# Kernel optimization log

Measured on AMD Instinct MI355X. Metric: run time of the kernel, lower is better.

## Reference

```python
import jax, jax.numpy as jnp
import numpy as np

BETA = 0.05      # temperature
BG_KNN = 50      # hard negatives per sample
N_CAMS = 6
C = 2000         # classes (proxies) per camera
D = 2048         # feature dim
B = 256          # batch size
MASK_VAL = -10000.0


def setup_inputs() -> dict:
    key = jax.random.key(0)
    k1, k2, k3, k4 = jax.random.split(key, 4)
    feats = jax.random.normal(k1, (B, D), jnp.float32)
    feats = feats / jnp.linalg.norm(feats, axis=1, keepdims=True)
    mem = jax.random.normal(k2, (N_CAMS, C, D), jnp.float32)
    mem = mem / jnp.linalg.norm(mem, axis=2, keepdims=True)
    cams = jax.random.randint(k3, (B,), 0, N_CAMS)
    labels = jax.random.randint(k4, (B,), 0, C)
    return {"features": feats, "memory": mem, "cams": cams, "labels": labels}


def _forward(features, memory, cams, labels):
    # Memory bank is non-differentiable in ExemplarMemory (grad only flows to inputs).
    mem_flat = jax.lax.stop_gradient(memory.reshape(N_CAMS * C, D))
    # [B, N_CAMS*C] similarities against the concatenated per-camera proxies (percam_tempV)
    sims_all = features @ mem_flat.T

    rows = jnp.arange(B)
    counts = jax.ops.segment_sum(jnp.ones((B,), sims_all.dtype), cams, num_segments=N_CAMS)
    safe_counts = jnp.maximum(counts, 1.0)

    # ---- per-camera proxy cross-entropy (ExemplarMemory forward + F.cross_entropy) ----
    # camera cc owns memory rows cc*C : (cc+1)*C; gather each sample's own-camera block
    block_idx = cams[:, None] * C + jnp.arange(C)[None, :]            # [B, C]
    percam_logits = jnp.take_along_axis(sims_all, block_idx, axis=1) / BETA
    ce = -jax.nn.log_softmax(percam_logits, axis=1)[rows, labels]     # [B]
    ce_sum = jax.ops.segment_sum(ce, cams, num_segments=N_CAMS)
    # original sums the per-camera *mean* CE over cameras present in the batch
    loss = jnp.sum(jnp.where(counts > 0, ce_sum / safe_counts, 0.0))

    # ---- cross-camera associate loss: positives + bg_knn hardest negatives ----
    # positives of label l live at global rows {j*C + l} for every camera j
    pos_idx = labels[:, None] + C * jnp.arange(N_CAMS)[None, :]       # [B, N_CAMS]
    temp_sims = jax.lax.stop_gradient(sims_all)
    temp_sims = temp_sims.at[rows[:, None], pos_idx].set(MASK_VAL)    # mask positives
    _, sel_idx = jax.lax.top_k(temp_sims, BG_KNN)                     # [B, BG_KNN] hard negs
    neg_logits = jnp.take_along_axis(sims_all, sel_idx, axis=1) / BETA
    pos_logits = jnp.take_along_axis(sims_all, pos_idx, axis=1) / BETA
    logits = jnp.concatenate([pos_logits, neg_logits], axis=1)       # [B, N_CAMS+BG_KNN]
    logsm = jax.nn.log_softmax(logits, axis=1)
    # soft target: uniform 1/n_pos mass on the positive slots
    assoc = -jnp.sum(logsm[:, :N_CAMS], axis=1) / N_CAMS              # [B]
    assoc_sum = jax.ops.segment_sum(assoc, cams, num_segments=N_CAMS)
    loss = loss + jnp.sum(jnp.where(counts > 0, 0.5 * assoc_sum / safe_counts, 0.0))
    return loss


def reference(features, memory, cams, labels):
    return _forward(features, memory, cams, labels)
```

## Files before the change

kernel.cpp:

```cpp
#include <hip/hip_runtime.h>
#include <hip/hip_bf16.h>
#include <math.h>

#define BETA_INV 20.0f
#define BG_KNN   50
#define N_CAMS   6
#define CLS      2000
#define DIM      2048
#define BATCH    256
#define NPROXY   (N_CAMS * CLS)
#define MASK_VAL -10000.0f
#define NKT      (DIM / 32)

typedef __attribute__((ext_vector_type(8))) short short8;
typedef __attribute__((ext_vector_type(4))) float f32x4;
typedef __attribute__((address_space(1))) const unsigned int g_u32;
typedef __attribute__((address_space(3))) unsigned int l_u32;

__device__ __forceinline__ uint2 cvt4(float4 v) {
    uint2 r;
    asm("v_cvt_pk_bf16_f32 %0, %1, %2" : "=v"(r.x) : "v"(v.x), "v"(v.y));
    asm("v_cvt_pk_bf16_f32 %0, %1, %2" : "=v"(r.y) : "v"(v.z), "v"(v.w));
    return r;
}

__global__ __launch_bounds__(256) void conv_t(const float* __restrict__ src,
                                              unsigned short* __restrict__ dst,
                                              int nrb)
{
    __shared__ unsigned short lds[32][72];
    const int t  = threadIdx.x;
    const int b  = blockIdx.x;
    const int rb = b % nrb, kb = b / nrb;
    const int r  = t >> 3, c8 = (t & 7) * 8;

    const float* sp = src + (size_t)(rb * 32 + r) * DIM + kb * 64 + c8;
    float4 f0 = *(const float4*)sp;
    float4 f1 = *(const float4*)(sp + 4);
    uint2 pa = cvt4(f0), pb = cvt4(f1);
    *(uint4*)&lds[r][c8] = make_uint4(pa.x, pa.y, pb.x, pb.y);
    __syncthreads();

    const int cidx = t >> 6;
    const int n16h = cidx >> 1, kth = cidx & 1;
    const int lane = t & 63;
    const int fr = lane & 15, kg = lane >> 4;
    uint4 v = *(const uint4*)&lds[n16h * 16 + fr][kth * 32 + kg * 8];
    const size_t N16 = (size_t)rb * 2 + n16h;
    const size_t KT  = (size_t)kb * 2 + kth;
    *(uint4*)(dst + ((N16 * NKT + KT) * 64 + lane) * 8) = v;
}

#define NSTEP 16

__global__ __launch_bounds__(512, 2) void gemm_fused(const unsigned short* __restrict__ At,
                                                     const float* __restrict__ Bm,
                                                     float* __restrict__ C)
{
    __shared__ __align__(16) unsigned short ldsA[2][16384];
    __shared__ __align__(16) float          ldsB[2][6144];

    const int tid = threadIdx.x;
    const int bid = blockIdx.x;
    const int bn  = (bid >> 1) * 96;
    const int kh  = bid & 1;

    const int lane = tid & 63, wid = tid >> 6;
    const int mw = wid >> 1;
    const int nw = wid & 1;
    const int fr = lane & 15, kg = lane >> 4;

    const unsigned short* pAq[4];
    int dA[4];
#pragma unroll
    for (int q = 0; q < 4; ++q) {
        int f = q * 512 + tid;
        int chunk = f >> 6, ln = f & 63;
        int n16 = chunk >> 1, ktl = chunk & 1;
        pAq[q] = At + ((size_t)(n16 * 64 + kh * 32 + ktl) * 64 + ln) * 8;
        dA[q] = f * 8;
    }
    const float* pBq[3];
    int dB[3];
#pragma unroll
    for (int q = 0; q < 3; ++q) {
        int f = q * 512 + tid;
        int row = f >> 4, c = f & 15;
        pBq[q] = Bm + (size_t)(bn + row) * DIM + kh * 1024 + ((c ^ (row & 15)) * 4);
        dB[q] = f * 4;
    }

#define STAGE(BUF, T) do {                                                                \
        _Pragma("unroll")                                                                 \
        for (int q = 0; q < 4; ++q)                                                       \
            __builtin_amdgcn_global_load_lds((g_u32*)(pAq[q] + (size_t)(T) * 1024),       \
                                             (l_u32*)&ldsA[BUF][dA[q]], 16, 0, 0);        \
        _Pragma("unroll")                                                                 \
        for (int q = 0; q < 3; ++q)                                                       \
            __builtin_amdgcn_global_load_lds((g_u32*)(pBq[q] + (size_t)(T) * 64),         \
                                             (l_u32*)&ldsB[BUF][dB[q]], 16, 0, 0);        \
    } while (0)

    f32x4 acc[4][3];
#pragma unroll
    for (int i = 0; i < 4; ++i)
#pragma unroll
        for (int j = 0; j < 3; ++j) acc[i][j] = (f32x4){0.f, 0.f, 0.f, 0.f};

#define COMPUTE(CUR) do {                                                                 \
    _Pragma("unroll")                                                                     \
    for (int ks = 0; ks < 2; ++ks) {                                                      \
        short8 bfr[3];                                                                    \
        _Pragma("unroll")                                                                 \
        for (int j = 0; j < 3; ++j) {                                                     \
            int row = nw * 48 + j * 16 + fr;                                              \
            int g0 = ks * 8 + kg * 2;                                                     \
            float4 lo = *(const float4*)&ldsB[CUR][row * 64 + ((g0 ^ fr) * 4)];           \
            float4 hi = *(const float4*)&ldsB[CUR][row * 64 + (((g0 + 1) ^ fr) * 4)];     \
            uint2 ca = cvt4(lo), cb = cvt4(hi);                                           \
            bfr[j] = __builtin_bit_cast(short8, make_uint4(ca.x, ca.y, cb.x, cb.y));      \
        }                                                                                 \
        _Pragma("unroll")                                                                 \
        for (int i = 0; i < 4; ++i) {                                                     \
            short8 af = *(const short8*)&ldsA[CUR][((mw * 4 + i) * 2 + ks) * 512 + lane * 8]; \
            _Pragma("unroll")                                                             \
            for (int j = 0; j < 3; ++j)                                                   \
                acc[i][j] = __builtin_amdgcn_mfma_f32_16x16x32_bf16(af, bfr[j], acc[i][j], 0, 0, 0); \
        }                                                                                 \
    }                                                                                     \
} while (0)

#define BODY(T, CUR, ISSUE, VMC) do {                                                     \
    __builtin_amdgcn_s_barrier();                   \
    __builtin_amdgcn_sched_barrier(0);                                                    \
    if (ISSUE) { STAGE((CUR) ^ 1, (T) + 1); }                                             \
    __builtin_amdgcn_sched_barrier(0);                                                    \
    asm volatile("s_waitcnt vmcnt(" VMC ")" ::: "memory");         \
    __builtin_amdgcn_sched_barrier(0);                                                    \
    __builtin_amdgcn_s_barrier();                           \
    __builtin_amdgcn_sched_barrier(0);                                                    \
    COMPUTE(CUR);                                                                         \
} while (0)

    STAGE(0, 0);
#pragma unroll 1
    for (int t = 0; t < NSTEP - 2; t += 2) {
        BODY(t,     0, 1, "7");
        BODY(t + 1, 1, 1, "7");
    }
    BODY(NSTEP - 2, 0, 1, "7");
    BODY(NSTEP - 1, 1, 0, "0");
#undef BODY
#undef COMPUTE
#undef STAGE

    float* Cp = C + (size_t)kh * BATCH * NPROXY;
#pragma unroll
    for (int i = 0; i < 4; ++i)
#pragma unroll
        for (int j = 0; j < 3; ++j)
#pragma unroll
            for (int r = 0; r < 4; ++r)
                Cp[(size_t)(mw * 64 + i * 16 + kg * 4 + r) * NPROXY + (bn + nw * 48 + j * 16 + fr)] = acc[i][j][r];
}

__device__ __forceinline__ float block_sum_f(float x, volatile float* red8, int lane, int wid) {
#pragma unroll
    for (int off = 32; off; off >>= 1) x += __shfl_xor(x, off);
    if (lane == 0) red8[wid] = x;
    __syncthreads();
    float t = 0.f;
#pragma unroll
    for (int w = 0; w < 8; ++w) t += red8[w];
    __syncthreads();
    return t;
}
__device__ __forceinline__ float block_max_f(float x, volatile float* red8, int lane, int wid) {
#pragma unroll
    for (int off = 32; off; off >>= 1) x = fmaxf(x, __shfl_xor(x, off));
    if (lane == 0) red8[wid] = x;
    __syncthreads();
    float t = -1e30f;
#pragma unroll
    for (int w = 0; w < 8; ++w) t = fmaxf(t, red8[w]);
    __syncthreads();
    return t;
}
__device__ __forceinline__ int block_sum_i(int x, volatile int* red8, int lane, int wid) {
#pragma unroll
    for (int off = 32; off; off >>= 1) x += __shfl_xor(x, off);
    if (lane == 0) red8[wid] = x;
    __syncthreads();
    int t = 0;
#pragma unroll
    for (int w = 0; w < 8; ++w) t += red8[w];
    __syncthreads();
    return t;
}

__global__ __launch_bounds__(512) void per_sample(const float* __restrict__ sims,
                                                  const int* __restrict__ cams,
                                                  const int* __restrict__ labels,
                                                  float* __restrict__ ce_out,
                                                  float* __restrict__ assoc_out)
{
    __shared__ float redf[8];
    __shared__ int   redi[8];
    __shared__ float pos_sh[N_CAMS];
    __shared__ float sh_vlab;

    const int i    = blockIdx.x;
    const int tid  = threadIdx.x;
    const int lane = tid & 63;
    const int wid  = tid >> 6;
    const float* s0 = sims + (size_t)i * NPROXY;
    const float* s1 = sims + (size_t)(BATCH + i) * NPROXY;
    const int cc   = cams[i];
    const int lab  = labels[i];

    float4 v[6];
#pragma unroll
    for (int ii = 0; ii < 6; ++ii) {
        int q = tid + 512 * ii;
        if (q < NPROXY / 4) {
            float4 a = *(const float4*)(s0 + 4 * q);
            float4 b = *(const float4*)(s1 + 4 * q);
            v[ii] = make_float4(a.x + b.x, a.y + b.y, a.z + b.z, a.w + b.w);
        } else v[ii] = make_float4(-1e30f, -1e30f, -1e30f, -1e30f);
    }

    const int plab = cc * CLS + lab;
    const int qlab = plab >> 2, clab = plab & 3;
#pragma unroll
    for (int ii = 0; ii < 6; ++ii) {
        if ((qlab >> 9) == ii && (qlab & 511) == tid) {
            float t = (clab == 0) ? v[ii].x : (clab == 1) ? v[ii].y : (clab == 2) ? v[ii].z : v[ii].w;
            sh_vlab = t;
        }
    }

    const int qlo = cc * 500, qhi = qlo + 500;
    float m = -1e30f;
#pragma unroll
    for (int ii = 0; ii < 6; ++ii) {
        int q = tid + 512 * ii;
        if (q >= qlo && q < qhi)
            m = fmaxf(m, fmaxf(fmaxf(v[ii].x, v[ii].y), fmaxf(v[ii].z, v[ii].w)));
    }
    const float smax = block_max_f(m, redf, lane, wid);
    float ls = 0.f;
#pragma unroll
    for (int ii = 0; ii < 6; ++ii) {
        int q = tid + 512 * ii;
        if (q >= qlo && q < qhi) {
            ls += __expf((v[ii].x - smax) * BETA_INV);
            ls += __expf((v[ii].y - smax) * BETA_INV);
            ls += __expf((v[ii].z - smax) * BETA_INV);
            ls += __expf((v[ii].w - smax) * BETA_INV);
        }
    }
    const float lsum = block_sum_f(ls, redf, lane, wid);
    if (tid == 0) ce_out[i] = logf(lsum) + (smax - sh_vlab) * BETA_INV;

#define DOPC(II, COMP, CIDX) { \
        int p = 4 * (tid + 512 * (II)) + (CIDX); \
        int r = p - lab; \
        if (r >= 0 && r <= (N_CAMS - 1) * CLS && (r % CLS) == 0) { \
            pos_sh[r / CLS] = v[II].COMP; \
            v[II].COMP = MASK_VAL; \
        } }
#pragma unroll
    for (int ii = 0; ii < 6; ++ii) {
        DOPC(ii, x, 0); DOPC(ii, y, 1); DOPC(ii, z, 2); DOPC(ii, w, 3);
    }
#undef DOPC
    __syncthreads();

    float mm = -1e30f;
#pragma unroll
    for (int ii = 0; ii < 6; ++ii)
        mm = fmaxf(mm, fmaxf(fmaxf(v[ii].x, v[ii].y), fmaxf(v[ii].z, v[ii].w)));
    const float M1 = block_max_f(mm, redf, lane, wid);

    float pmax = -1e30f, psum = 0.f;
#pragma unroll
    for (int j = 0; j < N_CAMS; ++j) {
        float pv = pos_sh[j];
        pmax = fmaxf(pmax, pv);
        psum += pv;
    }

    float lo = M1 - 0.5f, hi = M1 + 1e-4f;
    int cnt_hi = 0;
    for (int it = 0; it < 20; ++it) {
        const float mid = 0.5f * (lo + hi);
        int c = 0;
#pragma unroll
        for (int ii = 0; ii < 6; ++ii) {
            c += (v[ii].x >= mid); c += (v[ii].y >= mid);
            c += (v[ii].z >= mid); c += (v[ii].w >= mid);
        }
        const int tot = block_sum_i(c, redi, lane, wid);
        if (tot >= BG_KNN) lo = mid; else { hi = mid; cnt_hi = tot; }
    }

    const float M = fmaxf(M1, pmax);
    float ss = 0.f, vt = -1e30f;
#pragma unroll
    for (int ii = 0; ii < 6; ++ii) {
#define DOF(COMP) { float x = v[ii].COMP; \
        if (x >= hi) ss += __expf((x - M) * BETA_INV); \
        else if (x >= lo) vt = fmaxf(vt, x); }
        DOF(x) DOF(y) DOF(z) DOF(w)
#undef DOF
    }
    const float ssum = block_sum_f(ss, redf, lane, wid);
    const float vtie = block_max_f(vt, redf, lane, wid);

    if (tid == 0) {
        int need = BG_KNN - cnt_hi;
        float vts = (vtie < -1e29f) ? lo : vtie;
        float total = ssum + (float)need * __expf((vts - M) * BETA_INV);
#pragma unroll
        for (int j = 0; j < N_CAMS; ++j) total += __expf((pos_sh[j] - M) * BETA_INV);
        assoc_out[i] = M * BETA_INV + logf(total) - psum * BETA_INV / (float)N_CAMS;
    }
}

__global__ __launch_bounds__(256) void finalize(const int* __restrict__ cams,
                                                const float* __restrict__ ce,
                                                const float* __restrict__ assoc,
                                                float* __restrict__ out)
{
    __shared__ float ce_s[N_CAMS], as_s[N_CAMS];
    __shared__ int   cnt[N_CAMS];
    const int tid = threadIdx.x;
    if (tid < N_CAMS) { ce_s[tid] = 0.f; as_s[tid] = 0.f; cnt[tid] = 0; }
    __syncthreads();
    const int c = cams[tid];
    atomicAdd(&ce_s[c], ce[tid]);
    atomicAdd(&as_s[c], assoc[tid]);
    atomicAdd(&cnt[c], 1);
    __syncthreads();
    if (tid == 0) {
        float loss = 0.f;
        for (int k = 0; k < N_CAMS; ++k) {
            if (cnt[k] > 0) {
                float inv = 1.f / (float)cnt[k];
                loss += ce_s[k] * inv + 0.5f * as_s[k] * inv;
            }
        }
        out[0] = loss;
    }
}

extern "C" void kernel_launch(void* const* d_in, const int* in_sizes, int n_in,
                              void* d_out, int out_size, void* d_ws, size_t ws_size,
                              hipStream_t stream) {
    const float* feats  = (const float*)d_in[0];
    const float* mem    = (const float*)d_in[1];
    const int*   cams   = (const int*)d_in[2];
    const int*   labels = (const int*)d_in[3];
    float* out = (float*)d_out;

    float* sims  = (float*)d_ws;
    float* ce    = sims + (size_t)2 * BATCH * NPROXY;
    float* assoc = ce + BATCH;
    unsigned short* At = (unsigned short*)(assoc + BATCH);

    conv_t<<<(BATCH / 32) * (DIM / 64), 256, 0, stream>>>(feats, At, BATCH / 32);
    gemm_fused<<<250, 512, 0, stream>>>(At, mem, sims);
    per_sample<<<BATCH, 512, 0, stream>>>(sims, cams, labels, ce, assoc);
    finalize<<<1, 256, 0, stream>>>(cams, ce, assoc, out);
}
```

Baseline: 62.94 us.

## Switch GEMM to triple-buffered half-width K tiles and trim bisection iterations

```diff
diff --git a/kernel.cpp b/kernel.cpp
--- a/kernel.cpp
+++ b/kernel.cpp
@@ -51,14 +51,14 @@
     *(uint4*)(dst + ((N16 * NKT + KT) * 64 + lane) * 8) = v;
 }
 
-#define NSTEP 16
-
-__global__ __launch_bounds__(512, 2) void gemm_fused(const unsigned short* __restrict__ At,
-                                                     const float* __restrict__ Bm,
-                                                     float* __restrict__ C)
+#define NSTEP 32
+
+__global__ __launch_bounds__(512) void gemm_sk(const unsigned short* __restrict__ At,
+                                               const float* __restrict__ Bm,
+                                               float* __restrict__ C)
 {
-    __shared__ __align__(16) unsigned short ldsA[2][16384];
-    __shared__ __align__(16) float          ldsB[2][6144];
+    __shared__ __align__(16) unsigned short ldsA[3][8192];
+    __shared__ __align__(16) float          ldsB[3][3072];
 
     const int tid = threadIdx.x;
     const int bid = blockIdx.x;
@@ -69,87 +69,87 @@
     const int mw = wid >> 1;
     const int nw = wid & 1;
     const int fr = lane & 15, kg = lane >> 4;
-
-    const unsigned short* pAq[4];
-    int dA[4];
-#pragma unroll
-    for (int q = 0; q < 4; ++q) {
+    const int x7 = fr & 7;
+
+    const unsigned short* pAq[2];
+    int dA[2];
+#pragma unroll
+    for (int q = 0; q < 2; ++q) {
         int f = q * 512 + tid;
-        int chunk = f >> 6, ln = f & 63;
-        int n16 = chunk >> 1, ktl = chunk & 1;
-        pAq[q] = At + ((size_t)(n16 * 64 + kh * 32 + ktl) * 64 + ln) * 8;
+        int n16 = f >> 6, ln = f & 63;
+        pAq[q] = At + ((size_t)n16 * NKT + kh * 32) * 512 + ln * 8;
         dA[q] = f * 8;
     }
-    const float* pBq[3];
-    int dB[3];
-#pragma unroll
-    for (int q = 0; q < 3; ++q) {
+    const bool hasB2 = tid < 256;
+    const float* pBq[2];
+    int dB[2];
+#pragma unroll
+    for (int q = 0; q < 2; ++q) {
         int f = q * 512 + tid;
-        int row = f >> 4, c = f & 15;
-        pBq[q] = Bm + (size_t)(bn + row) * DIM + kh * 1024 + ((c ^ (row & 15)) * 4);
+        int row = f >> 3, c = f & 7;
+        pBq[q] = Bm + (size_t)(bn + row) * DIM + kh * 1024 + ((c ^ (row & 7)) * 4);
         dB[q] = f * 4;
     }
 
 #define STAGE(BUF, T) do {                                                                \
         _Pragma("unroll")                                                                 \
-        for (int q = 0; q < 4; ++q)                                                       \
-            __builtin_amdgcn_global_load_lds((g_u32*)(pAq[q] + (size_t)(T) * 1024),       \
+        for (int q = 0; q < 2; ++q)                                                       \
+            __builtin_amdgcn_global_load_lds((g_u32*)(pAq[q] + (size_t)(T) * 512),        \
                                              (l_u32*)&ldsA[BUF][dA[q]], 16, 0, 0);        \
+        __builtin_amdgcn_global_load_lds((g_u32*)(pBq[0] + (size_t)(T) * 32),             \
+                                         (l_u32*)&ldsB[BUF][dB[0]], 16, 0, 0);            \
+        if (hasB2)                                                                        \
+            __builtin_amdgcn_global_load_lds((g_u32*)(pBq[1] + (size_t)(T) * 32),         \
+                                             (l_u32*)&ldsB[BUF][dB[1]], 16, 0, 0);        \
+    } while (0)
+
+    f32x4 acc[4][3];
+#pragma unroll
+    for (int i = 0; i < 4; ++i)
+#pragma unroll
+        for (int j = 0; j < 3; ++j) acc[i][j] = (f32x4){0.f, 0.f, 0.f, 0.f};
+
+#define COMPUTE(CUR) do {                                                                 \
+    short8 af[4];                                                                         \
+    _Pragma("unroll")                                                                     \
+    for (int i = 0; i < 4; ++i)                                                           \
+        af[i] = *(const short8*)&ldsA[CUR][(mw * 4 + i) * 512 + lane * 8];                \
+    _Pragma("unroll")                                                                     \
+    for (int j = 0; j < 3; ++j) {                                                         \
+        int row = nw * 48 + j * 16 + fr;                                                  \
+        float4 lo = *(const float4*)&ldsB[CUR][row * 32 + (((kg * 2) ^ x7) * 4)];         \
+        float4 hi = *(const float4*)&ldsB[CUR][row * 32 + (((kg * 2 + 1) ^ x7) * 4)];     \
+        uint2 ca = cvt4(lo), cb = cvt4(hi);                                               \
+        short8 bf = __builtin_bit_cast(short8, make_uint4(ca.x, ca.y, cb.x, cb.y));       \
         _Pragma("unroll")                                                                 \
-        for (int q = 0; q < 3; ++q)                                                       \
-            __builtin_amdgcn_global_load_lds((g_u32*)(pBq[q] + (size_t)(T) * 64),         \
-                                             (l_u32*)&ldsB[BUF][dB[q]], 16, 0, 0);        \
-    } while (0)
-
-    f32x4 acc[4][3];
-#pragma unroll
-    for (int i = 0; i < 4; ++i)
-#pragma unroll
-        for (int j = 0; j < 3; ++j) acc[i][j] = (f32x4){0.f, 0.f, 0.f, 0.f};
-
-#define COMPUTE(CUR) do {                                                                 \
-    _Pragma("unroll")                                                                     \
-    for (int ks = 0; ks < 2; ++ks) {                                                      \
-        short8 bfr[3];                                                                    \
-        _Pragma("unroll")                                                                 \
-        for (int j = 0; j < 3; ++j) {                                                     \
-            int row = nw * 48 + j * 16 + fr;                                              \
-            int g0 = ks * 8 + kg * 2;                                                     \
-            float4 lo = *(const float4*)&ldsB[CUR][row * 64 + ((g0 ^ fr) * 4)];           \
-            float4 hi = *(const float4*)&ldsB[CUR][row * 64 + (((g0 + 1) ^ fr) * 4)];     \
-            uint2 ca = cvt4(lo), cb = cvt4(hi);                                           \
-            bfr[j] = __builtin_bit_cast(short8, make_uint4(ca.x, ca.y, cb.x, cb.y));      \
-        }                                                                                 \
-        _Pragma("unroll")                                                                 \
-        for (int i = 0; i < 4; ++i) {                                                     \
-            short8 af = *(const short8*)&ldsA[CUR][((mw * 4 + i) * 2 + ks) * 512 + lane * 8]; \
-            _Pragma("unroll")                                                             \
-            for (int j = 0; j < 3; ++j)                                                   \
-                acc[i][j] = __builtin_amdgcn_mfma_f32_16x16x32_bf16(af, bfr[j], acc[i][j], 0, 0, 0); \
-        }                                                                                 \
+        for (int i = 0; i < 4; ++i)                                                       \
+            acc[i][j] = __builtin_amdgcn_mfma_f32_16x16x32_bf16(af[i], bf, acc[i][j], 0, 0, 0); \
     }                                                                                     \
 } while (0)
 
-#define BODY(T, CUR, ISSUE, VMC) do {                                                     \
-    __builtin_amdgcn_s_barrier();                   \
+#define BODY(T, CUR, ISSUE, VX, VY) do {                                                  \
+    __builtin_amdgcn_s_barrier();                                                         \
     __builtin_amdgcn_sched_barrier(0);                                                    \
-    if (ISSUE) { STAGE((CUR) ^ 1, (T) + 1); }                                             \
+    if (ISSUE) { STAGE(((T) + 2) % 3, (T) + 2); }                                         \
     __builtin_amdgcn_sched_barrier(0);                                                    \
-    asm volatile("s_waitcnt vmcnt(" VMC ")" ::: "memory");         \
+    if (hasB2) asm volatile("s_waitcnt vmcnt(" VX ")" ::: "memory");                      \
+    else       asm volatile("s_waitcnt vmcnt(" VY ")" ::: "memory");                      \
     __builtin_amdgcn_sched_barrier(0);                                                    \
-    __builtin_amdgcn_s_barrier();                           \
+    __builtin_amdgcn_s_barrier();                                                         \
     __builtin_amdgcn_sched_barrier(0);                                                    \
     COMPUTE(CUR);                                                                         \
 } while (0)
 
     STAGE(0, 0);
+    STAGE(1, 1);
 #pragma unroll 1
-    for (int t = 0; t < NSTEP - 2; t += 2) {
-        BODY(t,     0, 1, "7");
-        BODY(t + 1, 1, 1, "7");
-    }
-    BODY(NSTEP - 2, 0, 1, "7");
-    BODY(NSTEP - 1, 1, 0, "0");
+    for (int t = 0; t < NSTEP - 2; t += 3) {
+        BODY(t,     0, 1, "8", "6");
+        BODY(t + 1, 1, 1, "8", "6");
+        BODY(t + 2, 2, 1, "8", "6");
+    }
+    BODY(NSTEP - 2, 0, 0, "4", "3");
+    BODY(NSTEP - 1, 1, 0, "0", "0");
 #undef BODY
 #undef COMPUTE
 #undef STAGE
@@ -292,7 +292,7 @@
 
     float lo = M1 - 0.5f, hi = M1 + 1e-4f;
     int cnt_hi = 0;
-    for (int it = 0; it < 20; ++it) {
+    for (int it = 0; it < 14; ++it) {
         const float mid = 0.5f * (lo + hi);
         int c = 0;
 #pragma unroll
@@ -369,7 +369,7 @@
     unsigned short* At = (unsigned short*)(assoc + BATCH);
 
     conv_t<<<(BATCH / 32) * (DIM / 64), 256, 0, stream>>>(feats, At, BATCH / 32);
-    gemm_fused<<<250, 512, 0, stream>>>(At, mem, sims);
+    gemm_sk<<<250, 512, 0, stream>>>(At, mem, sims);
     per_sample<<<BATCH, 512, 0, stream>>>(sims, cams, labels, ce, assoc);
     finalize<<<1, 256, 0, stream>>>(cams, ce, assoc, out);
 }
```

Measured after the change: 62.42 us. No clear change (-0.8%).
